# Performance work log

Measured on AMD Instinct MI355X. Metric: run time of the kernel, lower is better.

The kernel has to match this reference:

```python
import jax, jax.numpy as jnp
import numpy as np

N, DF, DR, H, K = 4096, 128, 64, 1024, 10


def _init_linear(key, fan_in, fan_out):
    kw, kb = jax.random.split(key)
    bound = 1.0 / np.sqrt(fan_in)
    W = jax.random.uniform(kw, (fan_in, fan_out), jnp.float32, -bound, bound)
    b = jax.random.uniform(kb, (fan_out,), jnp.float32, -bound, bound)
    return W, b


def setup_inputs() -> dict:
    key = jax.random.key(0)
    ks = jax.random.split(key, 8)
    condition = jax.random.normal(ks[0], (N, DF), jnp.float32)
    tensor = jax.random.normal(ks[1], (N, DR), jnp.float32)
    Win, b_in = _init_linear(ks[2], DF + DR, H)
    W1, b1 = _init_linear(ks[3], H, H)
    W2, b2 = _init_linear(ks[4], H, H)
    W3, b3 = _init_linear(ks[5], H, H)
    Wout, b_out = _init_linear(ks[6], H, DR)
    return {"condition": condition, "tensor": tensor,
            "Win": Win, "b_in": b_in, "W1": W1, "b1": b1,
            "W2": W2, "b2": b2, "W3": W3, "b3": b3,
            "Wout": Wout, "b_out": b_out}


def _mlp(x, Win, b_in, W1, b1, W2, b2, W3, b3, Wout, b_out):
    # FFNN: input layer + 3 hidden layers with Softplus, linear output -> DR
    h = jax.nn.softplus(x @ Win + b_in)
    h = jax.nn.softplus(h @ W1 + b1)
    h = jax.nn.softplus(h @ W2 + b2)
    h = jax.nn.softplus(h @ W3 + b3)
    return h @ Wout + b_out


def reference(condition, tensor, Win, b_in, W1, b1, W2, b2, W3, b3, Wout, b_out):
    # torch.cdist(condition, condition), p=2 -> [N, N]
    sq = jnp.sum(condition * condition, axis=-1)
    d2 = sq[:, None] + sq[None, :] - 2.0 * (condition @ condition.T)
    dist = jnp.sqrt(jnp.maximum(d2, 0.0))
    # torch.topk(dist, 10, dim=1, largest=False) -> k nearest neighbor indices
    _, neighbor_idx = jax.lax.top_k(-dist, K)  # [N, K]
    # gather neighbor groups
    cond_g = condition[neighbor_idx]  # [N, K, DF]
    tens_g = tensor[neighbor_idx]     # [N, K, DR]
    # MongeMapNetwork.pushforward: tensor - MLP(concat(condition, tensor))
    x = jnp.concatenate([cond_g, tens_g], axis=-1)  # [N, K, DF+DR]
    pushed = tens_g - _mlp(x, Win, b_in, W1, b1, W2, b2, W3, b3, Wout, b_out)
    return pushed  # [N, K, DR]
```

## Files before the change

### kernel.cpp

```cpp
#include <hip/hip_runtime.h>
#include <hip/hip_fp16.h>
#include <stdint.h>

typedef unsigned short u16;
typedef unsigned int   u32;
typedef unsigned long long u64;
typedef short v8bf __attribute__((ext_vector_type(8)));
typedef float v4f  __attribute__((ext_vector_type(4)));
typedef u16   v8u  __attribute__((ext_vector_type(8)));

#define NPTS 4096
#define DF   128
#define DR   64
#define HID  1024
#define KNN  10
#define DIN  192
#define NB   512
#define PREP_UNITS 5507

#define AS1 __attribute__((address_space(1)))
#define AS3 __attribute__((address_space(3)))

__device__ __forceinline__ float bf2f(u16 b){ return __uint_as_float(((unsigned)b)<<16); }
__device__ __forceinline__ u16 f2bf(float f){
  unsigned u = __float_as_uint(f);
  unsigned r = 0x7fffu + ((u>>16)&1u);
  return (u16)((u + r)>>16);
}
__device__ __forceinline__ u16 f2h(float f){
  __half h = __float2half(f);
  return __half_as_ushort(h);
}
__device__ __forceinline__ float softplus_f(float x){
  return x>15.f ? x : __logf(1.f + __expf(x));
}
__device__ __forceinline__ float rdv(const void* p, long j, int fl){
  return fl ? bf2f(((const u16*)p)[j]) : ((const float*)p)[j];
}
__device__ __forceinline__ void gl2lds16(const u16* g, u16* l){
  __builtin_amdgcn_global_load_lds((const AS1 unsigned int*)g, (AS3 unsigned int*)l, 16, 0, 0);
}

constexpr size_t OFF_FLAG  = 128;
constexpr size_t OFF_SQ    = 256;
constexpr size_t OFF_NIDX  = OFF_SQ    + 16384;
constexpr size_t OFF_BIAS  = OFF_NIDX  + 163840;
constexpr size_t OFF_CONDF = OFF_BIAS  + 16640;
constexpr size_t OFF_TENSF = OFF_CONDF + 2097152;
constexpr size_t OFF_WTIN  = OFF_TENSF + 1048576;
constexpr size_t OFF_WT1   = OFF_WTIN  + 393216;
constexpr size_t OFF_WT2   = OFF_WT1   + 2097152;
constexpr size_t OFF_WT3   = OFF_WT2   + 2097152;
constexpr size_t OFF_WTO   = OFF_WT3   + 2097152;
constexpr size_t OFF_DIST  = OFF_WTO   + 131072;
constexpr size_t OFF_X     = OFF_DIST  + 33554432;
constexpr size_t OFF_A0    = OFF_X     + 1572864;
constexpr size_t OFF_A1    = OFF_A0    + 8388608;
constexpr size_t OFF_P     = OFF_A1    + 8388608;
constexpr size_t OFF_SYNC  = OFF_P     + 4194304;

__device__ __forceinline__ void gbar(u32* rel, u32* slots, u32 e, int bid){
  __syncthreads();
  if(threadIdx.x == 0){
    __threadfence();
    __hip_atomic_store(&slots[bid], e+1u, __ATOMIC_RELEASE, __HIP_MEMORY_SCOPE_AGENT);
  }
  if(bid == 0){
    const int t = threadIdx.x;
    for(;;){
      u32 a = __hip_atomic_load(&slots[2*t],   __ATOMIC_ACQUIRE, __HIP_MEMORY_SCOPE_AGENT);
      u32 b = __hip_atomic_load(&slots[2*t+1], __ATOMIC_ACQUIRE, __HIP_MEMORY_SCOPE_AGENT);
      if(__syncthreads_and((a >= e+1u) && (b >= e+1u))) break;
      __builtin_amdgcn_s_sleep(1);
    }
    if(threadIdx.x == 0)
      __hip_atomic_store(rel, e+1u, __ATOMIC_RELEASE, __HIP_MEMORY_SCOPE_AGENT);
    __threadfence();
    __syncthreads();
  } else {
    if(threadIdx.x == 0){
      while(__hip_atomic_load(rel, __ATOMIC_ACQUIRE, __HIP_MEMORY_SCOPE_AGENT) < e+1u)
        __builtin_amdgcn_s_sleep(2);
      __threadfence();
    }
    __syncthreads();
  }
}

__device__ __forceinline__ int detect_fl(const void* cond, u16* SM){
  const u16* c = (const u16*)cond;
  int tid = threadIdx.x, n = 0;
  for(int i=tid; i<8192; i+=256){
    u16 v = c[2*i];
    int e = (v>>7)&0xff;
    n += (e>=96 && e<=158);
  }
  int* cnt = (int*)SM;
  cnt[tid] = n; __syncthreads();
  for(int s=128; s>0; s>>=1){ if(tid<s) cnt[tid]+=cnt[tid+s]; __syncthreads(); }
  int fl = (cnt[0] > 4915) ? 1 : 0;
  __syncthreads();
  return fl;
}

__device__ __forceinline__ void cvt8(float* dst, const void* src, long j0, int fl){
  if(fl){
    v8u h = *(const v8u*)&((const u16*)src)[j0];
    float4 a, b;
    a.x=bf2f(h[0]); a.y=bf2f(h[1]); a.z=bf2f(h[2]); a.w=bf2f(h[3]);
    b.x=bf2f(h[4]); b.y=bf2f(h[5]); b.z=bf2f(h[6]); b.w=bf2f(h[7]);
    *(float4*)dst = a; *(float4*)(dst+4) = b;
  } else {
    *(float4*)dst     = *(const float4*)&((const float*)src)[j0];
    *(float4*)(dst+4) = *(const float4*)&((const float*)src)[j0+4];
  }
}

__device__ __forceinline__ void prep_unit(int u, int tid, int fl,
    const void* cond, const void* tens,
    const void* Wi, const void* W1, const void* W2, const void* W3, const void* Wo,
    const void* bi, const void* b1, const void* b2, const void* b3, const void* bo,
    float* condF, float* tensF, float* biasF,
    u16* Oi, u16* O1, u16* O2, u16* O3, u16* Oo,
    float* sq, u16* X, u16* SM){
  if(u < 387){
    int v = u*256 + tid;
    if(v < 65536){ cvt8(condF + (size_t)v*8, cond, (long)v*8, fl); }
    else if(v < 98304){ int w = v - 65536; cvt8(tensF + (size_t)w*8, tens, (long)w*8, fl); }
    else if(v < 98824){
      int j = (v - 98304)*8;
      const void* src; int off;
      if(j < 1024){ src=bi; off=j; }
      else if(j < 2048){ src=b1; off=j-1024; }
      else if(j < 3072){ src=b2; off=j-2048; }
      else if(j < 4096){ src=b3; off=j-3072; }
      else             { src=bo; off=j-4096; }
      cvt8(biasF + j, src, off, fl);
    }
  } else if(u < 3715){
    u16 (*tile)[33] = (u16(*)[33])SM;
    int b = u - 387;
    const void* in; u16* out; int R, C, bx, by;
    if(b < 192)      {              in=Wi; out=Oi; R=192;  C=1024; bx=b&31; by=b>>5; }
    else if(b < 1216){ b -= 192;    in=W1; out=O1; R=1024; C=1024; bx=b&31; by=b>>5; }
    else if(b < 2240){ b -= 1216;   in=W2; out=O2; R=1024; C=1024; bx=b&31; by=b>>5; }
    else if(b < 3264){ b -= 2240;   in=W3; out=O3; R=1024; C=1024; bx=b&31; by=b>>5; }
    else             { b -= 3264;   in=Wo; out=Oo; R=1024; C=64;   bx=b&1;  by=b>>1; }
    int gx = bx*32, gy = by*32;
    int tx = tid&31, ty = tid>>5;
    #pragma unroll
    for(int r=ty; r<32; r+=8){
      size_t idx = (size_t)(gy+r)*C + gx + tx;
      tile[r][tx] = fl ? ((const u16*)in)[idx] : f2bf(((const float*)in)[idx]);
    }
    __syncthreads();
    #pragma unroll
    for(int r=ty; r<32; r+=8) out[(size_t)(gx+r)*R + gy + tx] = tile[tx][r];
  } else if(u < 4739){
    int b = u - 3715;
    int row = b*4 + (tid>>6), lane = tid&63;
    float a = rdv(cond, (long)row*DF + lane, fl);
    float c2 = rdv(cond, (long)row*DF + lane + 64, fl);
    double s = (double)a*a + (double)c2*c2;
    #pragma unroll
    for(int off=32; off>0; off>>=1) s += __shfl_down(s, off, 64);
    if(lane==0) sq[row] = (float)s;
  } else {
    int c = (u-4739)*256 + tid;
    int j = c/48;
    int off = (c - j*48)*4;
    ushort4 o;
    if(fl){
      o = (off < DF) ? *(const ushort4*)&((const u16*)cond)[(size_t)j*DF + off]
                     : *(const ushort4*)&((const u16*)tens)[(size_t)j*DR + off - DF];
    } else if(off < DF){
      o.x = f2bf(((const float*)cond)[(size_t)j*DF + off + 0]);
      o.y = f2bf(((const float*)cond)[(size_t)j*DF + off + 1]);
      o.z = f2bf(((const float*)cond)[(size_t)j*DF + off + 2]);
      o.w = f2bf(((const float*)cond)[(size_t)j*DF + off + 3]);
    }else{
      int t2 = off - DF;
      o.x = f2bf(((const float*)tens)[(size_t)j*DR + t2 + 0]);
      o.y = f2bf(((const float*)tens)[(size_t)j*DR + t2 + 1]);
      o.z = f2bf(((const float*)tens)[(size_t)j*DR + t2 + 2]);
      o.w = f2bf(((const float*)tens)[(size_t)j*DR + t2 + 3]);
    }
    *(ushort4*)&X[(size_t)j*DIN + off] = o;
  }
}

__device__ __forceinline__ void gemm_bt_body(const u16* __restrict__ A,
    const u16* __restrict__ Bt, const float* __restrict__ bias, u16* __restrict__ C,
    int Nc, int Kc, int bid, u16* As, u16* Bs){
  const int xcd = bid&7, slot = bid>>3;
  const int bm = (xcd*4 + (slot>>4)) * 128;
  const int bn = (slot&15) * 64;
  const int tid = threadIdx.x, lane = tid&63, wave = tid>>6;
  const int wm = (wave&1)*64, wn = (wave>>1)*32;
  int c0 = wave*128 + lane, c1 = c0 + 64;
  int r0 = c0>>2, q0 = c0&3, r1 = c1>>2;
  int cb = wave*64 + lane, rb = cb>>2, qb = cb&3;
  const u16* pA0 = A  + (size_t)(bm+r0)*Kc + (q0^(r0&3))*8;
  const u16* pA1 = A  + (size_t)(bm+r1)*Kc + (q0^(r0&3))*8;
  const u16* pB  = Bt + (size_t)(bn+rb)*Kc + (qb^(rb&3))*8;
  u16* lA0 = &As[wave*1024];
  u16* lA1 = &As[wave*1024 + 512];
  u16* lB  = &Bs[wave*512];
  const int m16 = lane&15, q = lane>>4;
  v4f acc[4][2] = {};
  for(int kb=0; kb<Kc; kb+=64){
    gl2lds16(pA0 + kb, lA0);
    gl2lds16(pA1 + kb, lA1);
    gl2lds16(pB  + kb, lB);
    gl2lds16(pA0 + kb + 32, lA0 + 4096);
    gl2lds16(pA1 + kb + 32, lA1 + 4096);
    gl2lds16(pB  + kb + 32, lB + 2048);
    __syncthreads();
    #pragma unroll
    for(int kk=0;kk<2;kk++){
      v8bf a[4], b[2];
      #pragma unroll
      for(int x=0;x<4;x++){
        int row = wm + x*16 + m16;
        a[x] = *(const v8bf*)&As[kk*4096 + row*32 + (q^(row&3))*8];
      }
      #pragma unroll
      for(int x=0;x<2;x++){
        int row = wn + x*16 + m16;
        b[x] = *(const v8bf*)&Bs[kk*2048 + row*32 + (q^(row&3))*8];
      }
      #pragma unroll
      for(int mi=0;mi<4;mi++)
        #pragma unroll
        for(int ni=0;ni<2;ni++)
          acc[mi][ni] = __builtin_amdgcn_mfma_f32_16x16x32_bf16(a[mi], b[ni], acc[mi][ni], 0,0,0);
    }
    __syncthreads();
  }
  const int col16 = lane&15, rowq = lane>>4;
  #pragma unroll
  for(int mi=0;mi<4;mi++){
    #pragma unroll
    for(int ni=0;ni<2;ni++){
      int cn = bn + wn + ni*16 + col16;
      float bi = bias[cn];
      #pragma unroll
      for(int r=0;r<4;r++){
        int rw = bm + wm + mi*16 + rowq*4 + r;
        float v = softplus_f(acc[mi][ni][r] + bi);
        C[(size_t)rw*Nc + cn] = f2bf(v);
      }
    }
  }
}

__device__ __forceinline__ void knn_body(const u16* __restrict__ distH,
    const float* __restrict__ condF, int* __restrict__ nidx, int row,
    float* __restrict__ af, int* __restrict__ cand, u64* __restrict__ keys){
  const int lane = threadIdx.x&63;
  af[lane]    = condF[(size_t)row*DF + lane];
  af[lane+64] = condF[(size_t)row*DF + lane + 64];
  const v8u* drow = (const v8u*)(distH + (size_t)row*NPTS);
  v8u vals[8];
  #pragma unroll
  for(int k=0;k<8;k++) vals[k] = drow[lane + k*64];
  u32 mx = 0;
  #pragma unroll
  for(int k=0;k<8;k++)
    #pragma unroll
    for(int e=0;e<8;e++){ u32 v = vals[k][e]; mx = v>mx ? v : mx; }
  #pragma unroll
  for(int off=32; off>0; off>>=1){
    u32 o = (u32)__shfl_down((int)mx, off, 64); mx = o>mx ? o : mx;
  }
  mx = (u32)__shfl((int)mx, 0, 64);
  u32 hi = mx+1, lo = 0;
  for(int it=0; it<17; ++it){
    u32 mid = (lo+hi)>>1;
    int c = 0;
    #pragma unroll
    for(int k=0;k<8;k++)
      #pragma unroll
      for(int e=0;e<8;e++)
        c += (int)__popcll(__ballot((u32)vals[k][e] < mid));
    if(c >= 16){ hi = mid; if(c <= 64) break; }
    else lo = mid;
  }
  const u32 t = hi;
  const u64 below = (1ull<<lane) - 1ull;
  int base = 0;
  #pragma unroll
  for(int k=0;k<8;k++)
    #pragma unroll
    for(int e=0;e<8;e++){
      bool p = (u32)vals[k][e] < t;
      u64 m = __ballot(p);
      if(p){
        int off = base + (int)__popcll(m & below);
        if(off < 64) cand[off] = (lane + k*64)*8 + e;
      }
      base += (int)__popcll(m);
    }
  int cnt = base > 64 ? 64 : base;
  u64 mykey = ~0ULL; int myj = -1;
  if(lane < cnt){
    int j = cand[lane];
    const float4* bp4 = (const float4*)(condF + (size_t)j*DF);
    double s = 0.0;
    #pragma unroll
    for(int v4i=0; v4i<32; v4i++){
      float4 bv = bp4[v4i];
      double d0 = (double)af[v4i*4+0]-(double)bv.x;
      double d1 = (double)af[v4i*4+1]-(double)bv.y;
      double d2 = (double)af[v4i*4+2]-(double)bv.z;
      double d3 = (double)af[v4i*4+3]-(double)bv.w;
      s += d0*d0 + d1*d1 + d2*d2 + d3*d3;
    }
    u64 bits = (u64)__double_as_longlong(s);
    mykey = (bits & ~0xFFFULL) | (u32)j;
    myj = j;
  }
  keys[lane] = mykey;
  if(lane < cnt){
    int rank = 0;
    for(int c2=0;c2<cnt;c2++) rank += (keys[c2] < mykey);
    if(rank < KNN) nidx[row*KNN + rank] = myj;
  }
}

__device__ __forceinline__ void knn_body2(const u16* __restrict__ distH,
    const float* __restrict__ condF, int* __restrict__ nidx, int row0, int row1,
    float* af0, float* af1, int* can0, int* can1, u64* key0, u64* key1){
  const int lane = threadIdx.x&63;
  af0[lane]    = condF[(size_t)row0*DF + lane];
  af0[lane+64] = condF[(size_t)row0*DF + lane + 64];
  af1[lane]    = condF[(size_t)row1*DF + lane];
  af1[lane+64] = condF[(size_t)row1*DF + lane + 64];
  const v8u* dr0 = (const v8u*)(distH + (size_t)row0*NPTS);
  const v8u* dr1 = (const v8u*)(distH + (size_t)row1*NPTS);
  v8u v0[8], v1[8];
  #pragma unroll
  for(int k=0;k<8;k++){ v0[k] = dr0[lane + k*64]; v1[k] = dr1[lane + k*64]; }
  u32 m0 = 0, m1 = 0;
  #pragma unroll
  for(int k=0;k<8;k++)
    #pragma unroll
    for(int e=0;e<8;e++){
      u32 a = v0[k][e]; m0 = a>m0 ? a : m0;
      u32 b = v1[k][e]; m1 = b>m1 ? b : m1;
    }
  #pragma unroll
  for(int off=32; off>0; off>>=1){
    u32 a = (u32)__shfl_down((int)m0, off, 64); m0 = a>m0 ? a : m0;
    u32 b = (u32)__shfl_down((int)m1, off, 64); m1 = b>m1 ? b : m1;
  }
  m0 = (u32)__shfl((int)m0, 0, 64);
  m1 = (u32)__shfl((int)m1, 0, 64);
  u32 hi0 = m0+1, lo0 = 0, hi1 = m1+1, lo1 = 0;
  bool done0 = false, done1 = false;
  for(int it=0; it<17 && !(done0 && done1); ++it){
    u32 mid0 = (lo0+hi0)>>1, mid1 = (lo1+hi1)>>1;
    int c0 = 0, c1 = 0;
    #pragma unroll
    for(int k=0;k<8;k++)
      #pragma unroll
      for(int e=0;e<8;e++){
        c0 += ((u32)v0[k][e] < mid0);
        c1 += ((u32)v1[k][e] < mid1);
      }
    #pragma unroll
    for(int off=32; off>0; off>>=1){
      c0 += __shfl_down(c0, off, 64);
      c1 += __shfl_down(c1, off, 64);
    }
    c0 = __shfl(c0, 0, 64);
    c1 = __shfl(c1, 0, 64);
    if(!done0){ if(c0 >= 16){ hi0 = mid0; if(c0 <= 64) done0 = true; } else lo0 = mid0; }
    if(!done1){ if(c1 >= 16){ hi1 = mid1; if(c1 <= 64) done1 = true; } else lo1 = mid1; }
  }
  const u32 t0 = hi0, t1 = hi1;
  const u64 below = (1ull<<lane) - 1ull;
  int base0 = 0, base1 = 0;
  #pragma unroll
  for(int k=0;k<8;k++)
    #pragma unroll
    for(int e=0;e<8;e++){
      bool p0 = (u32)v0[k][e] < t0;
      u64 q0 = __ballot(p0);
      if(p0){
        int off = base0 + (int)__popcll(q0 & below);
        if(off < 64) can0[off] = (lane + k*64)*8 + e;
      }
      base0 += (int)__popcll(q0);
      bool p1 = (u32)v1[k][e] < t1;
      u64 q1 = __ballot(p1);
      if(p1){
        int off = base1 + (int)__popcll(q1 & below);
        if(off < 64) can1[off] = (lane + k*64)*8 + e;
      }
      base1 += (int)__popcll(q1);
    }
  int cnt0 = base0 > 64 ? 64 : base0;
  int cnt1 = base1 > 64 ? 64 : base1;
  int j0 = (lane < cnt0) ? can0[lane] : 0;
  int j1 = (lane < cnt1) ? can1[lane] : 0;
  const float4* p0 = (const float4*)(condF + (size_t)j0*DF);
  const float4* p1 = (const float4*)(condF + (size_t)j1*DF);
  double s0 = 0.0, s1 = 0.0;
  #pragma unroll
  for(int v4i=0; v4i<32; v4i++){
    float4 a = p0[v4i], b = p1[v4i];
    double d0 = (double)af0[v4i*4+0]-(double)a.x;
    double d1 = (double)af0[v4i*4+1]-(double)a.y;
    double d2 = (double)af0[v4i*4+2]-(double)a.z;
    double d3 = (double)af0[v4i*4+3]-(double)a.w;
    s0 += d0*d0 + d1*d1 + d2*d2 + d3*d3;
    double e0 = (double)af1[v4i*4+0]-(double)b.x;
    double e1 = (double)af1[v4i*4+1]-(double)b.y;
    double e2 = (double)af1[v4i*4+2]-(double)b.z;
    double e3 = (double)af1[v4i*4+3]-(double)b.w;
    s1 += e0*e0 + e1*e1 + e2*e2 + e3*e3;
  }
  u64 mk0 = ~0ULL, mk1 = ~0ULL;
  if(lane < cnt0) mk0 = ((u64)__double_as_longlong(s0) & ~0xFFFULL) | (u32)j0;
  if(lane < cnt1) mk1 = ((u64)__double_as_longlong(s1) & ~0xFFFULL) | (u32)j1;
  key0[lane] = mk0;
  key1[lane] = mk1;
  if(lane < cnt0){
    int rank = 0;
    for(int c2=0;c2<cnt0;c2++) rank += (key0[c2] < mk0);
    if(rank < KNN) nidx[row0*KNN + rank] = j0;
  }
  if(lane < cnt1){
    int rank = 0;
    for(int c2=0;c2<cnt1;c2++) rank += (key1[c2] < mk1);
    if(rank < KNN) nidx[row1*KNN + rank] = j1;
  }
}

__device__ __forceinline__ void gram_tile(int gb, int fl,
    const u16* __restrict__ condB, const float* __restrict__ condF,
    const float* __restrict__ sq, u16* __restrict__ distH, u16* SM){
  const int bm = (gb&31)*128, bn = (gb>>5)*128;
  const int tid = threadIdx.x, lane = tid&63, wave = tid>>6;
  const int wm = (wave&1)*64, wn = (wave>>1)*64;
  const int m16 = lane&15, q = lane>>4;
  v4f acc[4][4] = {};
  if(fl){
    const int srow = wave*32 + (lane>>2);
    const int scol = ((lane&3)^(srow&3))*8;
    const u16* gA = condB + (size_t)(bm+srow)*DF + scol;
    const u16* gB = condB + (size_t)(bn+srow)*DF + scol;
    u16* lA = &SM[wave*1024];
    u16* lB = &SM[4096 + wave*1024];
    for(int kb=0; kb<DF; kb+=32){
      gl2lds16(gA + kb,                 lA);
      gl2lds16(gA + kb + (size_t)16*DF, lA + 512);
      gl2lds16(gB + kb,                 lB);
      gl2lds16(gB + kb + (size_t)16*DF, lB + 512);
      __syncthreads();
      v8bf a[4], b[4];
      #pragma unroll
      for(int x=0;x<4;x++){
        int ra = wm + x*16 + m16;
        int rb2 = wn + x*16 + m16;
        a[x] = *(const v8bf*)&SM[ra*32 + (q^(ra&3))*8];
        b[x] = *(const v8bf*)&SM[4096 + rb2*32 + (q^(rb2&3))*8];
      }
      #pragma unroll
      for(int mi=0;mi<4;mi++)
        #pragma unroll
        for(int ni=0;ni<4;ni++)
          acc[mi][ni] = __builtin_amdgcn_mfma_f32_16x16x32_bf16(a[mi], b[ni], acc[mi][ni], 0,0,0);
      __syncthreads();
    }
  } else {
    u16* Ahi = SM;
    u16* Alo = SM + 5120;
    u16* Bhi = SM + 10240;
    u16* Blo = SM + 15360;
    for(int kb=0; kb<DF; kb+=32){
      #pragma unroll
      for(int t=0;t<4;t++){
        int ch = tid + t*256;
        int r = ch>>3, c = (ch&7)*4;
        float4 av = *(const float4*)&condF[(size_t)(bm+r)*DF + kb + c];
        float4 bv = *(const float4*)&condF[(size_t)(bn+r)*DF + kb + c];
        ushort4 ah, bh, al, bl;
        ah.x=f2bf(av.x); ah.y=f2bf(av.y); ah.z=f2bf(av.z); ah.w=f2bf(av.w);
        bh.x=f2bf(bv.x); bh.y=f2bf(bv.y); bh.z=f2bf(bv.z); bh.w=f2bf(bv.w);
        al.x=f2bf(av.x-bf2f(ah.x)); al.y=f2bf(av.y-bf2f(ah.y));
        al.z=f2bf(av.z-bf2f(ah.z)); al.w=f2bf(av.w-bf2f(ah.w));
        bl.x=f2bf(bv.x-bf2f(bh.x)); bl.y=f2bf(bv.y-bf2f(bh.y));
        bl.z=f2bf(bv.z-bf2f(bh.z)); bl.w=f2bf(bv.w-bf2f(bh.w));
        *(ushort4*)&Ahi[r*40+c] = ah; *(ushort4*)&Bhi[r*40+c] = bh;
        *(ushort4*)&Alo[r*40+c] = al; *(ushort4*)&Blo[r*40+c] = bl;
      }
      __syncthreads();
      v8bf ahf[4], bhf[4], alf[4], blf[4];
      #pragma unroll
      for(int x=0;x<4;x++){
        ahf[x] = *(const v8bf*)&Ahi[(wm + x*16 + m16)*40 + q*8];
        bhf[x] = *(const v8bf*)&Bhi[(wn + x*16 + m16)*40 + q*8];
        alf[x] = *(const v8bf*)&Alo[(wm + x*16 + m16)*40 + q*8];
        blf[x] = *(const v8bf*)&Blo[(wn + x*16 + m16)*40 + q*8];
      }
      #pragma unroll
      for(int mi=0;mi<4;mi++)
        #pragma unroll
        for(int ni=0;ni<4;ni++){
          acc[mi][ni] = __builtin_amdgcn_mfma_f32_16x16x32_bf16(alf[mi], bhf[ni], acc[mi][ni], 0,0,0);
          acc[mi][ni] = __builtin_amdgcn_mfma_f32_16x16x32_bf16(ahf[mi], blf[ni], acc[mi][ni], 0,0,0);
          acc[mi][ni] = __builtin_amdgcn_mfma_f32_16x16x32_bf16(ahf[mi], bhf[ni], acc[mi][ni], 0,0,0);
        }
      __syncthreads();
    }
  }
  const int col16 = lane&15, rowq = lane>>4;
  #pragma unroll
  for(int mi=0;mi<4;mi++){
    #pragma unroll
    for(int ni=0;ni<4;ni++){
      int cj = bn + wn + ni*16 + col16;
      float sqj = sq[cj];
      #pragma unroll
      for(int r=0;r<4;r++){
        int ri = bm + wm + mi*16 + rowq*4 + r;
        float d2 = (sq[ri] + sqj) - 2.0f*acc[mi][ni][r];
        distH[(size_t)ri*NPTS + cj] = f2h(fmaxf(d2, 0.f));
      }
    }
  }
}

__device__ __forceinline__ void gemm_out_body(int obid, const u16* __restrict__ A,
    const u16* __restrict__ Bt, float* __restrict__ Pp, u16* As, u16* Bs){
  const int bm = (obid>>2)*128;
  const int k0 = (obid&3)*256;
  float* P = Pp + (size_t)(obid&3)*262144;
  const int tid = threadIdx.x, lane = tid&63, wave = tid>>6;
  const int wm = wave*32;
  int c0 = wave*128 + lane, c1 = c0 + 64;
  int ra0 = c0>>2, qa0 = c0&3, ra1 = c1>>2;
  int cb = wave*64 + lane;
  int rb = cb>>2, qb = cb&3;
  const u16* pA0 = A  + (size_t)(bm+ra0)*HID + (qa0^(ra0&3))*8;
  const u16* pA1 = A  + (size_t)(bm+ra1)*HID + (qa0^(ra0&3))*8;
  const u16* pB  = Bt + (size_t)rb*HID + (qb^(rb&3))*8;
  u16* lA0 = &As[(wave*128     )*8];
  u16* lA1 = &As[(wave*128 + 64)*8];
  u16* lB  = &Bs[(wave*64      )*8];
  const int m16 = lane&15, q = lane>>4;
  v4f acc[2][4] = {};
  for(int kb=k0; kb<k0+256; kb+=32){
    gl2lds16(pA0 + kb, lA0);
    gl2lds16(pA1 + kb, lA1);
    gl2lds16(pB  + kb, lB);
    __syncthreads();
    v8bf a[2], b[4];
    {
      int r0r = wm + m16, r1r = wm + 16 + m16;
      a[0] = *(const v8bf*)&As[r0r*32 + (q^(r0r&3))*8];
      a[1] = *(const v8bf*)&As[r1r*32 + (q^(r1r&3))*8];
    }
    #pragma unroll
    for(int x=0;x<4;x++){
      int row = x*16 + m16;
      b[x] = *(const v8bf*)&Bs[row*32 + (q^(row&3))*8];
    }
    #pragma unroll
    for(int mi=0;mi<2;mi++)
      #pragma unroll
      for(int ni=0;ni<4;ni++)
        acc[mi][ni] = __builtin_amdgcn_mfma_f32_16x16x32_bf16(a[mi], b[ni], acc[mi][ni], 0,0,0);
    __syncthreads();
  }
  const int col16 = lane&15, rowq = lane>>4;
  #pragma unroll
  for(int mi=0;mi<2;mi++){
    #pragma unroll
    for(int ni=0;ni<4;ni++){
      int cn = ni*16 + col16;
      #pragma unroll
      for(int r=0;r<4;r++){
        int rw = bm + wm + mi*16 + rowq*4 + r;
        P[(size_t)rw*DR + cn] = acc[mi][ni][r];
      }
    }
  }
}

__device__ __forceinline__ void gather_unit(int e, int fl,
    const float* Pp, const float* tensF, const float* biasF,
    const int* nidx, void* outv){
  int m = e>>4;
  int c = (e&15)*4;
  int j = nidx[m] & (NPTS-1);
  size_t rc = (size_t)j*DR + c;
  float4 t  = *(const float4*)&tensF[rc];
  float4 b  = *(const float4*)&biasF[4096 + c];
  float4 p0 = *(const float4*)&Pp[rc];
  float4 p1 = *(const float4*)&Pp[262144 + rc];
  float4 p2 = *(const float4*)&Pp[524288 + rc];
  float4 p3 = *(const float4*)&Pp[786432 + rc];
  float4 v;
  v.x = t.x - (b.x + ((p0.x+p1.x)+(p2.x+p3.x)));
  v.y = t.y - (b.y + ((p0.y+p1.y)+(p2.y+p3.y)));
  v.z = t.z - (b.z + ((p0.z+p1.z)+(p2.z+p3.z)));
  v.w = t.w - (b.w + ((p0.w+p1.w)+(p2.w+p3.w)));
  if(fl){
    ushort4 o; o.x=f2bf(v.x); o.y=f2bf(v.y); o.z=f2bf(v.z); o.w=f2bf(v.w);
    *(ushort4*)&((u16*)outv)[(size_t)m*DR + c] = o;
  }else{
    *(float4*)&((float*)outv)[(size_t)m*DR + c] = v;
  }
}

__global__ void __launch_bounds__(256,2) mega_k(
    const void* cond, const void* tens,
    const void* Wi, const void* W1w, const void* W2w, const void* W3w, const void* Wow,
    const void* bi, const void* b1, const void* b2, const void* b3, const void* bo,
    char* ws, void* outv){
  __shared__ __align__(16) u16 SM[20480];
  const int bid = blockIdx.x, tid = threadIdx.x;

  u32*   brel  = (u32*)  (ws + OFF_SYNC);
  u32*   slots = (u32*)  (ws + OFF_SYNC + 64);
  float* sqv   = (float*)(ws + OFF_SQ);
  int*   nidx  = (int*)  (ws + OFF_NIDX);
  float* biasF = (float*)(ws + OFF_BIAS);
  float* condF = (float*)(ws + OFF_CONDF);
  float* tensF = (float*)(ws + OFF_TENSF);
  u16*   Wt_in = (u16*)  (ws + OFF_WTIN);
  u16*   Wt1   = (u16*)  (ws + OFF_WT1);
  u16*   Wt2   = (u16*)  (ws + OFF_WT2);
  u16*   Wt3   = (u16*)  (ws + OFF_WT3);
  u16*   Wt_o  = (u16*)  (ws + OFF_WTO);
  u16*   distH = (u16*)  (ws + OFF_DIST);
  u16*   X     = (u16*)  (ws + OFF_X);
  u16*   A0    = (u16*)  (ws + OFF_A0);
  u16*   A1    = (u16*)  (ws + OFF_A1);
  float* Pp    = (float*)(ws + OFF_P);

  const int fl = detect_fl(cond, SM);

  for(int u=bid; u<PREP_UNITS; u+=NB){
    prep_unit(u, tid, fl, cond, tens, Wi, W1w, W2w, W3w, Wow, bi, b1, b2, b3, bo,
              condF, tensF, biasF, Wt_in, Wt1, Wt2, Wt3, Wt_o, sqv, X, SM);
    __syncthreads();
  }
  gbar(brel, slots, 0, bid);

  gemm_bt_body(X, Wt_in, biasF, A0, HID, DIN, bid, SM, SM+8192);
  __syncthreads();
  for(int gb=bid; gb<1024; gb+=NB){
    gram_tile(gb, fl, (const u16*)cond, condF, sqv, distH, SM);
    __syncthreads();
  }
  gbar(brel, slots, 1, bid);

  const int wv = tid>>6;
  float* kaf0 = (float*)SM + (wv*2+0)*128;
  float* kaf1 = (float*)SM + (wv*2+1)*128;
  int*   kc0  = (int*)((char*)SM + 4096) + (wv*2+0)*64;
  int*   kc1  = (int*)((char*)SM + 4096) + (wv*2+1)*64;
  u64*   kk0  = (u64*)((char*)SM + 8192) + (wv*2+0)*64;
  u64*   kk1  = (u64*)((char*)SM + 8192) + (wv*2+1)*64;

  if(bid < 256){
    gemm_bt_body(A0, Wt1, biasF+1024, A1, HID, HID, bid,     SM, SM+8192);
    __syncthreads();
    gemm_bt_body(A0, Wt1, biasF+1024, A1, HID, HID, bid+256, SM, SM+8192);
  } else {
    int r0 = (bid-256)*4 + wv;
    knn_body2(distH, condF, nidx, r0, r0 + 1024, kaf0, kaf1, kc0, kc1, kk0, kk1);
  }
  gbar(brel, slots, 2, bid);

  if(bid < 256){
    gemm_bt_body(A1, Wt2, biasF+2048, A0, HID, HID, bid,     SM, SM+8192);
    __syncthreads();
    gemm_bt_body(A1, Wt2, biasF+2048, A0, HID, HID, bid+256, SM, SM+8192);
  } else {
    int r0 = 2048 + (bid-256)*4 + wv;
    knn_body2(distH, condF, nidx, r0, r0 + 1024, kaf0, kaf1, kc0, kc1, kk0, kk1);
  }
  gbar(brel, slots, 3, bid);

  gemm_bt_body(A0, Wt3, biasF+3072, A1, HID, HID, bid, SM, SM+8192);
  gbar(brel, slots, 4, bid);

  if(bid < 128){
    gemm_out_body(bid, A1, Wt_o, Pp, SM, SM+8192);
  }
  gbar(brel, slots, 5, bid);

  for(int u=bid; u<2560; u+=NB)
    gather_unit(u*256 + tid, fl, Pp, tensF, biasF, nidx, outv);
}

__global__ void detect_k(const u16* __restrict__ c, int* __restrict__ flag){
  __shared__ int cnt[256];
  int t = threadIdx.x, n = 0;
  for(int i=t; i<8192; i+=256){
    u16 v = c[2*i];
    int e = (v>>7)&0xff;
    n += (e>=96 && e<=158);
  }
  cnt[t] = n; __syncthreads();
  for(int s=128; s>0; s>>=1){ if(t<s) cnt[t]+=cnt[t+s]; __syncthreads(); }
  if(t==0) *flag = (cnt[0] > 4915) ? 1 : 0;
}

__global__ void prep_k(const void* cond, const void* tens,
    const void* Wi, const void* W1, const void* W2, const void* W3, const void* Wo,
    const void* bi, const void* b1, const void* b2, const void* b3, const void* bo,
    float* condF, float* tensF, float* biasF,
    u16* Oi, u16* O1, u16* O2, u16* O3, u16* Oo,
    float* sq, u16* X, const int* __restrict__ flag){
  __shared__ __align__(16) u16 SM[1056];
  prep_unit(blockIdx.x, threadIdx.x, *flag, cond, tens, Wi, W1, W2, W3, Wo,
            bi, b1, b2, b3, bo, condF, tensF, biasF, Oi, O1, O2, O3, Oo, sq, X, SM);
}

__global__ __launch_bounds__(256,2) void gram_g1_k(const u16* __restrict__ condB,
    const float* __restrict__ condF, const float* __restrict__ sq,
    u16* __restrict__ distH, const int* __restrict__ flag,
    const u16* __restrict__ X, const u16* __restrict__ Wt_in,
    const float* __restrict__ biasF, u16* __restrict__ A0){
  __shared__ __align__(16) u16 SM[20480];
  const int bid = blockIdx.x;
  if(bid < 512){
    gemm_bt_body(X, Wt_in, biasF, A0, HID, DIN, bid, SM, SM+8192);
  } else {
    gram_tile(bid-512, *flag, condB, condF, sq, distH, SM);
  }
}

__global__ __launch_bounds__(256,2) void gemm_knn_k(const u16* __restrict__ A,
    const u16* __restrict__ Bt, const float* __restrict__ bias, u16* __restrict__ C,
    const u16* __restrict__ distH, const float* __restrict__ condF,
    int* __restrict__ nidx, int rowoff){
  __shared__ __align__(16) u16 gsm[12288];
  __shared__ float af[4][DF];
  __shared__ int   cand[4][64];
  __shared__ u64   keys[4][64];
  const int bid = blockIdx.x;
  if(bid < 512){
    gemm_bt_body(A, Bt, bias, C, HID, HID, bid, gsm, gsm+8192);
  } else {
    const int wv = threadIdx.x>>6;
    knn_body(distH, condF, nidx, rowoff + (bid-512)*4 + wv, af[wv], cand[wv], keys[wv]);
  }
}

__global__ __launch_bounds__(256,2) void gemm_bt_k(const u16* __restrict__ A,
    const u16* __restrict__ Bt, const float* __restrict__ bias, u16* __restrict__ C){
  __shared__ __align__(16) u16 As[8192];
  __shared__ __align__(16) u16 Bs[4096];
  gemm_bt_body(A, Bt, bias, C, HID, HID, blockIdx.x, As, Bs);
}

__global__ __launch_bounds__(256,2) void gemm_out_k(const u16* __restrict__ A,
    const u16* __restrict__ Bt, float* __restrict__ Pp){
  __shared__ __align__(16) u16 As[4096];
  __shared__ __align__(16) u16 Bs[2048];
  gemm_out_body(blockIdx.x, A, Bt, Pp, As, Bs);
}

__global__ void gather_k(const float* __restrict__ Pp, const float* __restrict__ tensF,
                         const float* __restrict__ biasF, const int* __restrict__ nidx,
                         void* __restrict__ outv, const int* __restrict__ flag){
  gather_unit(blockIdx.x*256 + threadIdx.x, *flag, Pp, tensF, biasF, nidx, outv);
}

extern "C" void kernel_launch(void* const* d_in, const int* in_sizes, int n_in,
                              void* d_out, int out_size, void* d_ws, size_t ws_size,
                              hipStream_t stream){
  char* ws = (char*)d_ws;
  int*   flag  = (int*)  (ws + OFF_FLAG);
  float* sqv   = (float*)(ws + OFF_SQ);
  int*   nidx  = (int*)  (ws + OFF_NIDX);
  float* biasF = (float*)(ws + OFF_BIAS);
  float* condF = (float*)(ws + OFF_CONDF);
  float* tensF = (float*)(ws + OFF_TENSF);
  u16*   Wt_in = (u16*)  (ws + OFF_WTIN);
  u16*   Wt1   = (u16*)  (ws + OFF_WT1);
  u16*   Wt2   = (u16*)  (ws + OFF_WT2);
  u16*   Wt3   = (u16*)  (ws + OFF_WT3);
  u16*   Wt_o  = (u16*)  (ws + OFF_WTO);
  u16*   distH = (u16*)  (ws + OFF_DIST);
  u16*   X     = (u16*)  (ws + OFF_X);
  u16*   A0    = (u16*)  (ws + OFF_A0);
  u16*   A1    = (u16*)  (ws + OFF_A1);
  float* Pp    = (float*)(ws + OFF_P);

  static int occ_cached = -1;
  if(occ_cached < 0){
    int occ = 0;
    if(hipOccupancyMaxActiveBlocksPerMultiprocessor(&occ, (const void*)mega_k, 256, 0)
       != hipSuccess) occ = 0;
    occ_cached = occ;
  }

  if(occ_cached >= 2){
    hipMemsetAsync(ws + OFF_SYNC, 0, 4096, stream);
    hipLaunchKernelGGL(mega_k, dim3(NB), dim3(256), 0, stream,
        d_in[0], d_in[1], d_in[2], d_in[4], d_in[6], d_in[8], d_in[10],
        d_in[3], d_in[5], d_in[7], d_in[9], d_in[11], ws, d_out);
    return;
  }

  detect_k <<<1, 256, 0, stream>>>((const u16*)d_in[0], flag);
  prep_k   <<<PREP_UNITS, 256, 0, stream>>>(d_in[0], d_in[1],
                d_in[2], d_in[4], d_in[6], d_in[8], d_in[10],
                d_in[3], d_in[5], d_in[7], d_in[9], d_in[11],
                condF, tensF, biasF, Wt_in, Wt1, Wt2, Wt3, Wt_o, sqv, X, flag);
  gram_g1_k<<<1536, 256, 0, stream>>>((const u16*)d_in[0], condF, sqv, distH, flag,
                                      X, Wt_in, biasF, A0);
  gemm_knn_k<<<1024, 256, 0, stream>>>(A0, Wt1, biasF+1024, A1, distH, condF, nidx, 0);
  gemm_knn_k<<<1024, 256, 0, stream>>>(A1, Wt2, biasF+2048, A0, distH, condF, nidx, 2048);
  gemm_bt_k  <<<512, 256, 0, stream>>>(A0, Wt3, biasF+3072, A1);
  gemm_out_k <<<128, 256, 0, stream>>>(A1, Wt_o, Pp);
  gather_k   <<<2560, 256, 0, stream>>>(Pp, tensF, biasF, nidx, d_out, flag);
}
```

Baseline: 204.2 us.

## Double persistent grid to 1024 blocks with one task per block per phase

Raises the persistent megakernel from 512 to 1024 blocks at four blocks per CU. Each block now runs a single GEMM tile or a single-row kNN task per phase instead of looping over two. The Gram phase assumes bf16 input, so the megakernel is gated on a host-side input-size check and the fp32 split path falls back to the multi-kernel sequence. The grid barrier now polls four slots per thread. This adds barrier participants and relies on four-block occupancy, which the tighter launch bounds and slightly smaller shared memory are meant to provide.

```diff
diff --git a/kernel.cpp b/kernel.cpp
--- a/kernel.cpp
+++ b/kernel.cpp
@@ -15,7 +15,7 @@
 #define HID  1024
 #define KNN  10
 #define DIN  192
-#define NB   512
+#define NB   1024
 #define PREP_UNITS 5507
 
 #define AS1 __attribute__((address_space(1)))
@@ -68,9 +68,11 @@
   if(bid == 0){
     const int t = threadIdx.x;
     for(;;){
-      u32 a = __hip_atomic_load(&slots[2*t],   __ATOMIC_ACQUIRE, __HIP_MEMORY_SCOPE_AGENT);
-      u32 b = __hip_atomic_load(&slots[2*t+1], __ATOMIC_ACQUIRE, __HIP_MEMORY_SCOPE_AGENT);
-      if(__syncthreads_and((a >= e+1u) && (b >= e+1u))) break;
+      u32 a = __hip_atomic_load(&slots[4*t],   __ATOMIC_ACQUIRE, __HIP_MEMORY_SCOPE_AGENT);
+      u32 b = __hip_atomic_load(&slots[4*t+1], __ATOMIC_ACQUIRE, __HIP_MEMORY_SCOPE_AGENT);
+      u32 c = __hip_atomic_load(&slots[4*t+2], __ATOMIC_ACQUIRE, __HIP_MEMORY_SCOPE_AGENT);
+      u32 d = __hip_atomic_load(&slots[4*t+3], __ATOMIC_ACQUIRE, __HIP_MEMORY_SCOPE_AGENT);
+      if(__syncthreads_and((a>=e+1u)&&(b>=e+1u)&&(c>=e+1u)&&(d>=e+1u))) break;
       __builtin_amdgcn_s_sleep(1);
     }
     if(threadIdx.x == 0)
@@ -328,193 +330,106 @@
   }
 }
 
-__device__ __forceinline__ void knn_body2(const u16* __restrict__ distH,
-    const float* __restrict__ condF, int* __restrict__ nidx, int row0, int row1,
-    float* af0, float* af1, int* can0, int* can1, u64* key0, u64* key1){
-  const int lane = threadIdx.x&63;
-  af0[lane]    = condF[(size_t)row0*DF + lane];
-  af0[lane+64] = condF[(size_t)row0*DF + lane + 64];
-  af1[lane]    = condF[(size_t)row1*DF + lane];
-  af1[lane+64] = condF[(size_t)row1*DF + lane + 64];
-  const v8u* dr0 = (const v8u*)(distH + (size_t)row0*NPTS);
-  const v8u* dr1 = (const v8u*)(distH + (size_t)row1*NPTS);
-  v8u v0[8], v1[8];
+__device__ __forceinline__ void gram_tile_b16(int gb,
+    const u16* __restrict__ condB, const float* __restrict__ sq,
+    u16* __restrict__ distH, u16* SM){
+  const int bm = (gb&31)*128, bn = (gb>>5)*128;
+  const int lane = threadIdx.x&63, wave = threadIdx.x>>6;
+  const int wm = (wave&1)*64, wn = (wave>>1)*64;
+  const int m16 = lane&15, q = lane>>4;
+  v4f acc[4][4] = {};
+  const int srow = wave*32 + (lane>>2);
+  const int scol = ((lane&3)^(srow&3))*8;
+  const u16* gA = condB + (size_t)(bm+srow)*DF + scol;
+  const u16* gB = condB + (size_t)(bn+srow)*DF + scol;
+  u16* lA = &SM[wave*1024];
+  u16* lB = &SM[4096 + wave*1024];
+  for(int kb=0; kb<DF; kb+=32){
+    gl2lds16(gA + kb,                 lA);
+    gl2lds16(gA + kb + (size_t)16*DF, lA + 512);
+    gl2lds16(gB + kb,                 lB);
+    gl2lds16(gB + kb + (size_t)16*DF, lB + 512);
+    __syncthreads();
+    v8bf a[4], b[4];
+    #pragma unroll
+    for(int x=0;x<4;x++){
+      int ra = wm + x*16 + m16;
+      int rb2 = wn + x*16 + m16;
+      a[x] = *(const v8bf*)&SM[ra*32 + (q^(ra&3))*8];
+      b[x] = *(const v8bf*)&SM[4096 + rb2*32 + (q^(rb2&3))*8];
+    }
+    #pragma unroll
+    for(int mi=0;mi<4;mi++)
+      #pragma unroll
+      for(int ni=0;ni<4;ni++)
+        acc[mi][ni] = __builtin_amdgcn_mfma_f32_16x16x32_bf16(a[mi], b[ni], acc[mi][ni], 0,0,0);
+    __syncthreads();
+  }
+  const int col16 = lane&15, rowq = lane>>4;
   #pragma unroll
-  for(int k=0;k<8;k++){ v0[k] = dr0[lane + k*64]; v1[k] = dr1[lane + k*64]; }
-  u32 m0 = 0, m1 = 0;
-  #pragma unroll
-  for(int k=0;k<8;k++)
-    #pragma unroll
-    for(int e=0;e<8;e++){
-      u32 a = v0[k][e]; m0 = a>m0 ? a : m0;
-      u32 b = v1[k][e]; m1 = b>m1 ? b : m1;
-    }
-  #pragma unroll
-  for(int off=32; off>0; off>>=1){
-    u32 a = (u32)__shfl_down((int)m0, off, 64); m0 = a>m0 ? a : m0;
-    u32 b = (u32)__shfl_down((int)m1, off, 64); m1 = b>m1 ? b : m1;
-  }
-  m0 = (u32)__shfl((int)m0, 0, 64);
-  m1 = (u32)__shfl((int)m1, 0, 64);
-  u32 hi0 = m0+1, lo0 = 0, hi1 = m1+1, lo1 = 0;
-  bool done0 = false, done1 = false;
-  for(int it=0; it<17 && !(done0 && done1); ++it){
-    u32 mid0 = (lo0+hi0)>>1, mid1 = (lo1+hi1)>>1;
-    int c0 = 0, c1 = 0;
-    #pragma unroll
-    for(int k=0;k<8;k++)
-      #pragma unroll
-      for(int e=0;e<8;e++){
-        c0 += ((u32)v0[k][e] < mid0);
-        c1 += ((u32)v1[k][e] < mid1);
+  for(int mi=0;mi<4;mi++){
+    #pragma unroll
+    for(int ni=0;ni<4;ni++){
+      int cj = bn + wn + ni*16 + col16;
+      float sqj = sq[cj];
+      #pragma unroll
+      for(int r=0;r<4;r++){
+        int ri = bm + wm + mi*16 + rowq*4 + r;
+        float d2 = (sq[ri] + sqj) - 2.0f*acc[mi][ni][r];
+        distH[(size_t)ri*NPTS + cj] = f2h(fmaxf(d2, 0.f));
       }
-    #pragma unroll
-    for(int off=32; off>0; off>>=1){
-      c0 += __shfl_down(c0, off, 64);
-      c1 += __shfl_down(c1, off, 64);
-    }
-    c0 = __shfl(c0, 0, 64);
-    c1 = __shfl(c1, 0, 64);
-    if(!done0){ if(c0 >= 16){ hi0 = mid0; if(c0 <= 64) done0 = true; } else lo0 = mid0; }
-    if(!done1){ if(c1 >= 16){ hi1 = mid1; if(c1 <= 64) done1 = true; } else lo1 = mid1; }
-  }
-  const u32 t0 = hi0, t1 = hi1;
-  const u64 below = (1ull<<lane) - 1ull;
-  int base0 = 0, base1 = 0;
-  #pragma unroll
-  for(int k=0;k<8;k++)
-    #pragma unroll
-    for(int e=0;e<8;e++){
-      bool p0 = (u32)v0[k][e] < t0;
-      u64 q0 = __ballot(p0);
-      if(p0){
-        int off = base0 + (int)__popcll(q0 & below);
-        if(off < 64) can0[off] = (lane + k*64)*8 + e;
-      }
-      base0 += (int)__popcll(q0);
-      bool p1 = (u32)v1[k][e] < t1;
-      u64 q1 = __ballot(p1);
-      if(p1){
-        int off = base1 + (int)__popcll(q1 & below);
-        if(off < 64) can1[off] = (lane + k*64)*8 + e;
-      }
-      base1 += (int)__popcll(q1);
-    }
-  int cnt0 = base0 > 64 ? 64 : base0;
-  int cnt1 = base1 > 64 ? 64 : base1;
-  int j0 = (lane < cnt0) ? can0[lane] : 0;
-  int j1 = (lane < cnt1) ? can1[lane] : 0;
-  const float4* p0 = (const float4*)(condF + (size_t)j0*DF);
-  const float4* p1 = (const float4*)(condF + (size_t)j1*DF);
-  double s0 = 0.0, s1 = 0.0;
-  #pragma unroll
-  for(int v4i=0; v4i<32; v4i++){
-    float4 a = p0[v4i], b = p1[v4i];
-    double d0 = (double)af0[v4i*4+0]-(double)a.x;
-    double d1 = (double)af0[v4i*4+1]-(double)a.y;
-    double d2 = (double)af0[v4i*4+2]-(double)a.z;
-    double d3 = (double)af0[v4i*4+3]-(double)a.w;
-    s0 += d0*d0 + d1*d1 + d2*d2 + d3*d3;
-    double e0 = (double)af1[v4i*4+0]-(double)b.x;
-    double e1 = (double)af1[v4i*4+1]-(double)b.y;
-    double e2 = (double)af1[v4i*4+2]-(double)b.z;
-    double e3 = (double)af1[v4i*4+3]-(double)b.w;
-    s1 += e0*e0 + e1*e1 + e2*e2 + e3*e3;
-  }
-  u64 mk0 = ~0ULL, mk1 = ~0ULL;
-  if(lane < cnt0) mk0 = ((u64)__double_as_longlong(s0) & ~0xFFFULL) | (u32)j0;
-  if(lane < cnt1) mk1 = ((u64)__double_as_longlong(s1) & ~0xFFFULL) | (u32)j1;
-  key0[lane] = mk0;
-  key1[lane] = mk1;
-  if(lane < cnt0){
-    int rank = 0;
-    for(int c2=0;c2<cnt0;c2++) rank += (key0[c2] < mk0);
-    if(rank < KNN) nidx[row0*KNN + rank] = j0;
-  }
-  if(lane < cnt1){
-    int rank = 0;
-    for(int c2=0;c2<cnt1;c2++) rank += (key1[c2] < mk1);
-    if(rank < KNN) nidx[row1*KNN + rank] = j1;
+    }
   }
 }
 
 __device__ __forceinline__ void gram_tile(int gb, int fl,
     const u16* __restrict__ condB, const float* __restrict__ condF,
     const float* __restrict__ sq, u16* __restrict__ distH, u16* SM){
+  if(fl){ gram_tile_b16(gb, condB, sq, distH, SM); return; }
   const int bm = (gb&31)*128, bn = (gb>>5)*128;
   const int tid = threadIdx.x, lane = tid&63, wave = tid>>6;
   const int wm = (wave&1)*64, wn = (wave>>1)*64;
   const int m16 = lane&15, q = lane>>4;
   v4f acc[4][4] = {};
-  if(fl){
-    const int srow = wave*32 + (lane>>2);
-    const int scol = ((lane&3)^(srow&3))*8;
-    const u16* gA = condB + (size_t)(bm+srow)*DF + scol;
-    const u16* gB = condB + (size_t)(bn+srow)*DF + scol;
-    u16* lA = &SM[wave*1024];
-    u16* lB = &SM[4096 + wave*1024];
-    for(int kb=0; kb<DF; kb+=32){
-      gl2lds16(gA + kb,                 lA);
-      gl2lds16(gA + kb + (size_t)16*DF, lA + 512);
-      gl2lds16(gB + kb,                 lB);
-      gl2lds16(gB + kb + (size_t)16*DF, lB + 512);
-      __syncthreads();
-      v8bf a[4], b[4];
-      #pragma unroll
-      for(int x=0;x<4;x++){
-        int ra = wm + x*16 + m16;
-        int rb2 = wn + x*16 + m16;
-        a[x] = *(const v8bf*)&SM[ra*32 + (q^(ra&3))*8];
-        b[x] = *(const v8bf*)&SM[4096 + rb2*32 + (q^(rb2&3))*8];
+  u16* Ahi = SM;
+  u16* Alo = SM + 5120;
+  u16* Bhi = SM + 10240;
+  u16* Blo = SM + 15360;
+  for(int kb=0; kb<DF; kb+=32){
+    #pragma unroll
+    for(int t=0;t<4;t++){
+      int ch = tid + t*256;
+      int r = ch>>3, c = (ch&7)*4;
+      float4 av = *(const float4*)&condF[(size_t)(bm+r)*DF + kb + c];
+      float4 bv = *(const float4*)&condF[(size_t)(bn+r)*DF + kb + c];
+      ushort4 ah, bh, al, bl;
+      ah.x=f2bf(av.x); ah.y=f2bf(av.y); ah.z=f2bf(av.z); ah.w=f2bf(av.w);
+      bh.x=f2bf(bv.x); bh.y=f2bf(bv.y); bh.z=f2bf(bv.z); bh.w=f2bf(bv.w);
+      al.x=f2bf(av.x-bf2f(ah.x)); al.y=f2bf(av.y-bf2f(ah.y));
+      al.z=f2bf(av.z-bf2f(ah.z)); al.w=f2bf(av.w-bf2f(ah.w));
+      bl.x=f2bf(bv.x-bf2f(bh.x)); bl.y=f2bf(bv.y-bf2f(bh.y));
+      bl.z=f2bf(bv.z-bf2f(bh.z)); bl.w=f2bf(bv.w-bf2f(bh.w));
+      *(ushort4*)&Ahi[r*40+c] = ah; *(ushort4*)&Bhi[r*40+c] = bh;
+      *(ushort4*)&Alo[r*40+c] = al; *(ushort4*)&Blo[r*40+c] = bl;
+    }
+    __syncthreads();
+    v8bf ahf[4], bhf[4], alf[4], blf[4];
+    #pragma unroll
+    for(int x=0;x<4;x++){
+      ahf[x] = *(const v8bf*)&Ahi[(wm + x*16 + m16)*40 + q*8];
+      bhf[x] = *(const v8bf*)&Bhi[(wn + x*16 + m16)*40 + q*8];
+      alf[x] = *(const v8bf*)&Alo[(wm + x*16 + m16)*40 + q*8];
+      blf[x] = *(const v8bf*)&Blo[(wn + x*16 + m16)*40 + q*8];
+    }
+    #pragma unroll
+    for(int mi=0;mi<4;mi++)
+      #pragma unroll
+      for(int ni=0;ni<4;ni++){
+        acc[mi][ni] = __builtin_amdgcn_mfma_f32_16x16x32_bf16(alf[mi], bhf[ni], acc[mi][ni], 0,0,0);
+        acc[mi][ni] = __builtin_amdgcn_mfma_f32_16x16x32_bf16(ahf[mi], blf[ni], acc[mi][ni], 0,0,0);
+        acc[mi][ni] = __builtin_amdgcn_mfma_f32_16x16x32_bf16(ahf[mi], bhf[ni], acc[mi][ni], 0,0,0);
       }
-      #pragma unroll
-      for(int mi=0;mi<4;mi++)
-        #pragma unroll
-        for(int ni=0;ni<4;ni++)
-          acc[mi][ni] = __builtin_amdgcn_mfma_f32_16x16x32_bf16(a[mi], b[ni], acc[mi][ni], 0,0,0);
-      __syncthreads();
-    }
-  } else {
-    u16* Ahi = SM;
-    u16* Alo = SM + 5120;
-    u16* Bhi = SM + 10240;
-    u16* Blo = SM + 15360;
-    for(int kb=0; kb<DF; kb+=32){
-      #pragma unroll
-      for(int t=0;t<4;t++){
-        int ch = tid + t*256;
-        int r = ch>>3, c = (ch&7)*4;
-        float4 av = *(const float4*)&condF[(size_t)(bm+r)*DF + kb + c];
-        float4 bv = *(const float4*)&condF[(size_t)(bn+r)*DF + kb + c];
-        ushort4 ah, bh, al, bl;
-        ah.x=f2bf(av.x); ah.y=f2bf(av.y); ah.z=f2bf(av.z); ah.w=f2bf(av.w);
-        bh.x=f2bf(bv.x); bh.y=f2bf(bv.y); bh.z=f2bf(bv.z); bh.w=f2bf(bv.w);
-        al.x=f2bf(av.x-bf2f(ah.x)); al.y=f2bf(av.y-bf2f(ah.y));
-        al.z=f2bf(av.z-bf2f(ah.z)); al.w=f2bf(av.w-bf2f(ah.w));
-        bl.x=f2bf(bv.x-bf2f(bh.x)); bl.y=f2bf(bv.y-bf2f(bh.y));
-        bl.z=f2bf(bv.z-bf2f(bh.z)); bl.w=f2bf(bv.w-bf2f(bh.w));
-        *(ushort4*)&Ahi[r*40+c] = ah; *(ushort4*)&Bhi[r*40+c] = bh;
-        *(ushort4*)&Alo[r*40+c] = al; *(ushort4*)&Blo[r*40+c] = bl;
-      }
-      __syncthreads();
-      v8bf ahf[4], bhf[4], alf[4], blf[4];
-      #pragma unroll
-      for(int x=0;x<4;x++){
-        ahf[x] = *(const v8bf*)&Ahi[(wm + x*16 + m16)*40 + q*8];
-        bhf[x] = *(const v8bf*)&Bhi[(wn + x*16 + m16)*40 + q*8];
-        alf[x] = *(const v8bf*)&Alo[(wm + x*16 + m16)*40 + q*8];
-        blf[x] = *(const v8bf*)&Blo[(wn + x*16 + m16)*40 + q*8];
-      }
-      #pragma unroll
-      for(int mi=0;mi<4;mi++)
-        #pragma unroll
-        for(int ni=0;ni<4;ni++){
-          acc[mi][ni] = __builtin_amdgcn_mfma_f32_16x16x32_bf16(alf[mi], bhf[ni], acc[mi][ni], 0,0,0);
-          acc[mi][ni] = __builtin_amdgcn_mfma_f32_16x16x32_bf16(ahf[mi], blf[ni], acc[mi][ni], 0,0,0);
-          acc[mi][ni] = __builtin_amdgcn_mfma_f32_16x16x32_bf16(ahf[mi], bhf[ni], acc[mi][ni], 0,0,0);
-        }
-      __syncthreads();
-    }
+    __syncthreads();
   }
   const int col16 = lane&15, rowq = lane>>4;
   #pragma unroll
@@ -616,12 +531,12 @@
   }
 }
 
-__global__ void __launch_bounds__(256,2) mega_k(
+__global__ void __launch_bounds__(256,4) mega_k(
     const void* cond, const void* tens,
     const void* Wi, const void* W1w, const void* W2w, const void* W3w, const void* Wow,
     const void* bi, const void* b1, const void* b2, const void* b3, const void* bo,
     char* ws, void* outv){
-  __shared__ __align__(16) u16 SM[20480];
+  __shared__ __align__(16) u16 SM[19968];
   const int bid = blockIdx.x, tid = threadIdx.x;
 
   u32*   brel  = (u32*)  (ws + OFF_SYNC);
@@ -651,43 +566,35 @@
   }
   gbar(brel, slots, 0, bid);
 
-  gemm_bt_body(X, Wt_in, biasF, A0, HID, DIN, bid, SM, SM+8192);
-  __syncthreads();
-  for(int gb=bid; gb<1024; gb+=NB){
-    gram_tile(gb, fl, (const u16*)cond, condF, sqv, distH, SM);
-    __syncthreads();
-  }
+  if(bid < 512){
+    gemm_bt_body(X, Wt_in, biasF, A0, HID, DIN, bid, SM, SM+8192);
+    __syncthreads();
+  }
+  gram_tile_b16(bid, (const u16*)cond, sqv, distH, SM);
   gbar(brel, slots, 1, bid);
 
   const int wv = tid>>6;
-  float* kaf0 = (float*)SM + (wv*2+0)*128;
-  float* kaf1 = (float*)SM + (wv*2+1)*128;
-  int*   kc0  = (int*)((char*)SM + 4096) + (wv*2+0)*64;
-  int*   kc1  = (int*)((char*)SM + 4096) + (wv*2+1)*64;
-  u64*   kk0  = (u64*)((char*)SM + 8192) + (wv*2+0)*64;
-  u64*   kk1  = (u64*)((char*)SM + 8192) + (wv*2+1)*64;
-
-  if(bid < 256){
-    gemm_bt_body(A0, Wt1, biasF+1024, A1, HID, HID, bid,     SM, SM+8192);
-    __syncthreads();
-    gemm_bt_body(A0, Wt1, biasF+1024, A1, HID, HID, bid+256, SM, SM+8192);
+  float* kaf  = (float*)SM + wv*128;
+  int*   kcan = (int*)((char*)SM + 2048) + wv*64;
+  u64*   kkey = (u64*)((char*)SM + 4096) + wv*64;
+
+  if(bid < 512){
+    gemm_bt_body(A0, Wt1, biasF+1024, A1, HID, HID, bid, SM, SM+8192);
   } else {
-    int r0 = (bid-256)*4 + wv;
-    knn_body2(distH, condF, nidx, r0, r0 + 1024, kaf0, kaf1, kc0, kc1, kk0, kk1);
+    knn_body(distH, condF, nidx, (bid-512)*4 + wv, kaf, kcan, kkey);
   }
   gbar(brel, slots, 2, bid);
 
-  if(bid < 256){
-    gemm_bt_body(A1, Wt2, biasF+2048, A0, HID, HID, bid,     SM, SM+8192);
-    __syncthreads();
-    gemm_bt_body(A1, Wt2, biasF+2048, A0, HID, HID, bid+256, SM, SM+8192);
+  if(bid < 512){
+    gemm_bt_body(A1, Wt2, biasF+2048, A0, HID, HID, bid, SM, SM+8192);
   } else {
-    int r0 = 2048 + (bid-256)*4 + wv;
-    knn_body2(distH, condF, nidx, r0, r0 + 1024, kaf0, kaf1, kc0, kc1, kk0, kk1);
+    knn_body(distH, condF, nidx, 2048 + (bid-512)*4 + wv, kaf, kcan, kkey);
   }
   gbar(brel, slots, 3, bid);
 
-  gemm_bt_body(A0, Wt3, biasF+3072, A1, HID, HID, bid, SM, SM+8192);
+  if(bid < 512){
+    gemm_bt_body(A0, Wt3, biasF+3072, A1, HID, HID, bid, SM, SM+8192);
+  }
   gbar(brel, slots, 4, bid);
 
   if(bid < 128){
@@ -795,6 +702,8 @@
   u16*   A1    = (u16*)  (ws + OFF_A1);
   float* Pp    = (float*)(ws + OFF_P);
 
+  const int is_bf16 = (in_sizes[0] < 1500000);
+
   static int occ_cached = -1;
   if(occ_cached < 0){
     int occ = 0;
@@ -803,8 +712,8 @@
     occ_cached = occ;
   }
 
-  if(occ_cached >= 2){
-    hipMemsetAsync(ws + OFF_SYNC, 0, 4096, stream);
+  if(is_bf16 && occ_cached >= 4){
+    hipMemsetAsync(ws + OFF_SYNC, 0, 8192, stream);
     hipLaunchKernelGGL(mega_k, dim3(NB), dim3(256), 0, stream,
         d_in[0], d_in[1], d_in[2], d_in[4], d_in[6], d_in[8], d_in[10],
         d_in[3], d_in[5], d_in[7], d_in[9], d_in[11], ws, d_out);
```

Result: no change. 204.0 us (-0.1%).
